# Kernel optimization log

Hardware: AMD Instinct MI355X
Metric: run time of the kernel (lower is better)

Reference implementation:

```python
import jax, jax.numpy as jnp
import numpy as np

EPS = 1e-5
GROUPS = 8
OUT_PLANES = 256
GP = OUT_PLANES // GROUPS  # group_planes = 32


def _bn_eval(x, p, ch_axis):
    # p: [4, C] = (gamma, beta, running_mean, running_var); eval-mode batchnorm
    shape = [1] * x.ndim
    shape[ch_axis] = -1
    g, b, m, v = (p[i].reshape(shape) for i in range(4))
    return g * (x - m) * jax.lax.rsqrt(v + EPS) + b


def _make_bn(key, ch):
    k1, k2, k3, k4 = jax.random.split(key, 4)
    gamma = jax.random.uniform(k1, (ch,)) + 0.5
    beta = jax.random.normal(k2, (ch,)) * 0.1
    mean = jax.random.normal(k3, (ch,)) * 0.1
    var = jax.random.uniform(k4, (ch,)) + 0.5
    return jnp.stack([gamma, beta, mean, var])  # [4, ch]


def setup_inputs() -> dict:
    key = jax.random.key(0)
    ks = jax.random.split(key, 6)
    N, C, D, Hh, Ww = 1, 256, 16, 32, 64
    x = jax.random.normal(ks[0], (N, C, D, Hh, Ww), dtype=jnp.float32)
    # qkv 1x1 conv weight: [out_planes*2, in_planes]
    qkv_w = jax.random.normal(ks[1], (OUT_PLANES * 2, C), dtype=jnp.float32) * np.sqrt(1.0 / C)
    # relative positional table: [group_planes*2, 2*H-1]
    relative = jax.random.normal(ks[2], (GP * 2, 2 * Ww - 1), dtype=jnp.float32) * np.sqrt(1.0 / GP)
    bn_qkv = _make_bn(ks[3], OUT_PLANES * 2)
    bn_sim = _make_bn(ks[4], GROUPS * 3)
    bn_out = _make_bn(ks[5], OUT_PLANES * 2)
    return {"x": x, "qkv_w": qkv_w, "relative": relative,
            "bn_qkv": bn_qkv, "bn_sim": bn_sim, "bn_out": bn_out}


def reference(x, qkv_w, relative, bn_qkv, bn_sim, bn_out):
    N, C, D, Hh, Ww = x.shape
    G, OP, gp = GROUPS, OUT_PLANES, GP
    # width == 0: permute(0,2,3,1,4) -> [N, D, Hh, C, Ww]; attend along Ww
    xp = jnp.transpose(x, (0, 2, 3, 1, 4))
    H = Ww
    B = N * D * Hh
    xr = xp.reshape(B, C, H)
    # 1x1 conv + BN over channels
    qkv = jnp.einsum('oc,bch->boh', qkv_w, xr)
    qkv = _bn_eval(qkv, bn_qkv, 1)
    qkv = qkv.reshape(B, G, 2 * gp, H)
    q = qkv[:, :, : gp // 2]          # [B,G,gp/2,H]
    k = qkv[:, :, gp // 2: gp]        # [B,G,gp/2,H]
    v = qkv[:, :, gp:]                # [B,G,gp,H]
    # relative-position gather: emb[c,i,j] = relative[c, i-j+H-1]
    idx = jnp.arange(H)[:, None] - jnp.arange(H)[None, :] + H - 1  # [H,H]
    emb = relative[:, idx]            # [2*gp, H, H]
    q_e = emb[: gp // 2]
    k_e = emb[gp // 2: gp]
    v_e = emb[gp:]
    qr = jnp.einsum('bgci,cij->bgij', q, q_e)
    kr = jnp.einsum('bgci,cij->bgji', k, k_e)  # einsum + transpose(2,3) fused
    qk = jnp.einsum('bgci,bgcj->bgij', q, k)
    sim = jnp.concatenate([qk, qr, kr], axis=1)  # [B, 3G, H, H]
    sim = _bn_eval(sim, bn_sim, 1)
    sim = sim.reshape(B, 3, G, H, H).sum(axis=1)
    sim = jax.nn.softmax(sim, axis=3)
    sv = jnp.einsum('bgij,bgcj->bgci', sim, v)
    sve = jnp.einsum('bgij,cij->bgci', sim, v_e)
    so = jnp.concatenate([sv, sve], axis=-1).reshape(B, 2 * OP, H)
    out = _bn_eval(so, bn_out, 1)
    out = out.reshape(N, D, Hh, OP, 2, H).sum(axis=-2)
    out = jnp.transpose(out, (0, 3, 1, 2, 4))  # [N, OP, D, Hh, Ww]
    return out
```

## Files before the change

### kernel.cpp

```cpp
#include <hip/hip_runtime.h>

#define EPS 1e-5f

typedef _Float16 half4_t __attribute__((ext_vector_type(4)));
typedef _Float16 half8_t __attribute__((ext_vector_type(8)));
typedef float floatx4 __attribute__((ext_vector_type(4)));

__device__ __forceinline__ unsigned short f2hb(float f) {
  _Float16 h = (_Float16)f;
  return __builtin_bit_cast(unsigned short, h);
}
__device__ __forceinline__ float hb2f(unsigned short u) {
  return (float)__builtin_bit_cast(_Float16, u);
}
__device__ __forceinline__ unsigned int pack2(float a, float b) {
  return (unsigned int)f2hb(a) | ((unsigned int)f2hb(b) << 16);
}

#define WS_QKT 16777216
#define WS_WH 33554432
#define WS_RELTQ 33816576
#define WS_RELTK 33820672
#define WS_RELV 33824768
#define WS_BNSF 33832960
#define WS_BNOSC 33833088
#define WS_BNOSH 33835136
#define WS_BNQSC 33837184
#define WS_BNQSH 33839232

__global__ __launch_bounds__(256) void k_prep(const float* __restrict__ W,
                                              const float* __restrict__ bnq,
                                              const float* __restrict__ rel,
                                              const float* __restrict__ bns,
                                              const float* __restrict__ bno,
                                              char* __restrict__ ws) {
  const int bid = blockIdx.x, tid = threadIdx.x;
  if (bid < 8) {
    unsigned short* Wh = (unsigned short*)(ws + WS_WH);
    const int base = bid * 16384;
#pragma unroll
    for (int u = 0; u < 16; ++u) {
      const int i = base + u * 1024 + tid * 4;
      const float4 v = *reinterpret_cast<const float4*>(&W[i]);
      uint2 p;
      p.x = pack2(v.x, v.y);
      p.y = pack2(v.z, v.w);
      *reinterpret_cast<uint2*>(&Wh[i]) = p;
    }
  } else {
    unsigned short* relTq = (unsigned short*)(ws + WS_RELTQ);
    unsigned short* relTk = (unsigned short*)(ws + WS_RELTK);
    unsigned short* relV = (unsigned short*)(ws + WS_RELV);
    float* bnsF = (float*)(ws + WS_BNSF);
    float* bnoSc = (float*)(ws + WS_BNOSC);
    float* bnoSh = (float*)(ws + WS_BNOSH);
    float* bnqSc = (float*)(ws + WS_BNQSC);
    float* bnqSh = (float*)(ws + WS_BNQSH);
    for (int idx = tid; idx < 2048; idx += 256) {
      const int t = idx >> 4, c = idx & 15;
      relTq[idx] = (t < 127) ? f2hb(rel[c * 127 + t]) : (unsigned short)0;
      relTk[idx] = (t < 127) ? f2hb(rel[(16 + c) * 127 + t]) : (unsigned short)0;
    }
    for (int idx = tid; idx < 4096; idx += 256) {
      const int c = idx >> 7, t = idx & 127;
      relV[idx] = (t < 127) ? f2hb(rel[(32 + c) * 127 + t]) : (unsigned short)0;
    }
    if (tid < 8) {
      const int g = tid;
      const float scA = bns[g] / sqrtf(bns[72 + g] + EPS);
      const float scB = bns[8 + g] / sqrtf(bns[72 + 8 + g] + EPS);
      const float scC = bns[16 + g] / sqrtf(bns[72 + 16 + g] + EPS);
      const float shv = (bns[24 + g] - bns[48 + g] * scA) +
                        (bns[24 + 8 + g] - bns[48 + 8 + g] * scB) +
                        (bns[24 + 16 + g] - bns[48 + 16 + g] * scC);
      bnsF[g * 4 + 0] = scA;
      bnsF[g * 4 + 1] = scB;
      bnsF[g * 4 + 2] = scC;
      bnsF[g * 4 + 3] = shv;
    }
    for (int idx = tid; idx < 512; idx += 256) {
      const float sc = bno[idx] / sqrtf(bno[1536 + idx] + EPS);
      bnoSc[idx] = sc;
      bnoSh[idx] = bno[512 + idx] - bno[1024 + idx] * sc;
      const float qc = bnq[idx] / sqrtf(bnq[1536 + idx] + EPS);
      bnqSc[idx] = qc;
      bnqSh[idx] = bnq[512 + idx] - bnq[1024 + idx] * qc;
    }
  }
}

__global__ __launch_bounds__(512, 4) void k_qkv(const float* __restrict__ x,
                                                char* __restrict__ ws) {
  const unsigned short* Wh = (const unsigned short*)(ws + WS_WH);
  const float* bnqSc = (const float*)(ws + WS_BNQSC);
  const float* bnqSh = (const float*)(ws + WS_BNQSH);
  unsigned short* qkv_h = (unsigned short*)ws;
  unsigned short* qkT = (unsigned short*)(ws + WS_QKT);
  __shared__ __align__(16) char arena[36864];
  unsigned short* xT = (unsigned short*)arena;
  unsigned short* qk_t = (unsigned short*)arena;

  const int tid = threadIdx.x;
  const int lane = tid & 63;
  const int w = tid >> 6;
  const int l15 = lane & 15, kg = lane >> 4;
  const size_t b = blockIdx.x;
  const int n0g = (int)b * 64;

  {
    const int k = tid >> 1;
    const int nb = (tid & 1) * 32;
    const float* src = x + (size_t)k * 32768 + n0g + nb;
    unsigned short hv[32];
#pragma unroll
    for (int u = 0; u < 8; ++u) {
      const float4 v4 = *reinterpret_cast<const float4*>(src + u * 4);
      hv[u * 4 + 0] = f2hb(v4.x);
      hv[u * 4 + 1] = f2hb(v4.y);
      hv[u * 4 + 2] = f2hb(v4.z);
      hv[u * 4 + 3] = f2hb(v4.w);
    }
#pragma unroll
    for (int e = 0; e < 32; ++e) xT[(nb + e) * 280 + k] = hv[e];
  }
  __syncthreads();

  floatx4 acc[4][4] = {};
#pragma unroll
  for (int kk = 0; kk < 8; ++kk) {
    half8_t af[4], bf[4];
#pragma unroll
    for (int fm = 0; fm < 4; ++fm)
      af[fm] = *reinterpret_cast<const half8_t*>(Wh + (size_t)(w * 64 + fm * 16 + l15) * 256 +
                                                 kk * 32 + kg * 8);
#pragma unroll
    for (int fn = 0; fn < 4; ++fn)
      bf[fn] = *reinterpret_cast<const half8_t*>(xT + (fn * 16 + l15) * 280 + kk * 32 + kg * 8);
#pragma unroll
    for (int fm = 0; fm < 4; ++fm)
#pragma unroll
      for (int fn = 0; fn < 4; ++fn)
        acc[fm][fn] = __builtin_amdgcn_mfma_f32_16x16x32_f16(af[fm], bf[fn], acc[fm][fn], 0, 0, 0);
  }
  __syncthreads();

  const int o0 = w * 64;
#pragma unroll
  for (int fm = 0; fm < 4; ++fm) {
    const float4 sc4 = *reinterpret_cast<const float4*>(&bnqSc[o0 + fm * 16 + kg * 4]);
    const float4 sh4 = *reinterpret_cast<const float4*>(&bnqSh[o0 + fm * 16 + kg * 4]);
#pragma unroll
    for (int fn = 0; fn < 4; ++fn) {
      const int h = fn * 16 + l15;
      const float v0 = fmaf(acc[fm][fn][0], sc4.x, sh4.x);
      const float v1 = fmaf(acc[fm][fn][1], sc4.y, sh4.y);
      const float v2 = fmaf(acc[fm][fn][2], sc4.z, sh4.z);
      const float v3 = fmaf(acc[fm][fn][3], sc4.w, sh4.w);
      if (fm < 2) {
        uint2 p;
        p.x = pack2(v0, v1);
        p.y = pack2(v2, v3);
        *reinterpret_cast<uint2*>(&qk_t[w * 2304 + h * 36 + fm * 16 + kg * 4]) = p;
      } else {
        const int cb = (fm - 2) * 16 + kg * 4;
        unsigned short* dst = &qkv_h[((b * 8 + w) * 32 + cb) * 64 + h];
        dst[0] = f2hb(v0);
        dst[64] = f2hb(v1);
        dst[128] = f2hb(v2);
        dst[192] = f2hb(v3);
      }
    }
  }
  __syncthreads();
#pragma unroll
  for (int it = 0; it < 4; ++it) {
    const int idx = it * 512 + tid;
    const int g2 = idx >> 8, e = idx & 255;
    const int h = e >> 2, c0 = (e & 3) * 8;
    const unsigned short* srcp = &qk_t[g2 * 2304 + h * 36 + c0];
    const uint2 a = *reinterpret_cast<const uint2*>(srcp);
    const uint2 b2 = *reinterpret_cast<const uint2*>(srcp + 4);
    uint4 wv;
    wv.x = a.x;
    wv.y = a.y;
    wv.z = b2.x;
    wv.w = b2.y;
    *reinterpret_cast<uint4*>(&qkT[((b * 8 + g2) * 64 + h) * 32 + c0]) = wv;
  }
}

#define QKS 36
#define PBS 72
#define PPS 136

__global__ __launch_bounds__(256, 4) void k_attn(const char* __restrict__ ws,
                                                 float* __restrict__ out) {
  const unsigned short* qkv_h = (const unsigned short*)ws;
  const unsigned short* qkTg = (const unsigned short*)(ws + WS_QKT);
  const unsigned short* relTq = (const unsigned short*)(ws + WS_RELTQ);
  const unsigned short* relTk = (const unsigned short*)(ws + WS_RELTK);
  const unsigned short* relV = (const unsigned short*)(ws + WS_RELV);
  const float* bnsF = (const float*)(ws + WS_BNSF);
  const float* bnoSc = (const float*)(ws + WS_BNOSC);
  const float* bnoSh = (const float*)(ws + WS_BNOSH);

  __shared__ __align__(16) char arena[32768];
  unsigned short* qkL = (unsigned short*)arena;
  unsigned short* M1T = (unsigned short*)arena;
  unsigned short* M2T = (unsigned short*)(arena + 16384);
  unsigned short* Pb = (unsigned short*)arena;
  unsigned short* Pp = (unsigned short*)(arena + 9216);
  unsigned short* Vb = (unsigned short*)(arena + 26624);
  float* rowsumL = (float*)(arena + 31232);

  const int tid = threadIdx.x;
  const int lane = tid & 63;
  const int wid = tid >> 6;
  const int l15 = lane & 15, kg = lane >> 4;
  const int bg = blockIdx.x;
  const int b = bg >> 3, g = bg & 7;

  {
    const uint4 qv =
        *reinterpret_cast<const uint4*>(&qkTg[(size_t)(((b << 3) + g)) * 2048 + tid * 8]);
    const int i = tid >> 2, c0 = (tid & 3) * 8;
    uint2 lo, hi;
    lo.x = qv.x;
    lo.y = qv.y;
    hi.x = qv.z;
    hi.y = qv.w;
    *reinterpret_cast<uint2*>(&qkL[i * QKS + c0]) = lo;
    *reinterpret_cast<uint2*>(&qkL[i * QKS + c0 + 4]) = hi;
  }
  __syncthreads();

  const half4_t aq = *reinterpret_cast<const half4_t*>(&qkL[(wid * 16 + l15) * QKS + kg * 4]);
  const half4_t ak =
      *reinterpret_cast<const half4_t*>(&qkL[(wid * 16 + l15) * QKS + 16 + kg * 4]);
  half4_t bqr[4];
#pragma unroll
  for (int nt = 0; nt < 4; ++nt)
    bqr[nt] = *reinterpret_cast<const half4_t*>(&qkL[(nt * 16 + l15) * QKS + 16 + kg * 4]);
  __syncthreads();

  floatx4 qkreg[4];
  {
    half4_t brq[8], brk[8];
#pragma unroll
    for (int nt = 0; nt < 8; ++nt) {
      brq[nt] = *reinterpret_cast<const half4_t*>(&relTq[(nt * 16 + l15) * 16 + kg * 4]);
      brk[nt] = *reinterpret_cast<const half4_t*>(&relTk[(nt * 16 + l15) * 16 + kg * 4]);
    }
    __builtin_amdgcn_s_setprio(1);
#pragma unroll
    for (int nt = 0; nt < 4; ++nt) {
      const floatx4 z = {};
      qkreg[nt] = __builtin_amdgcn_mfma_f32_16x16x16f16(aq, bqr[nt], z, 0, 0, 0);
    }
    const int mcol = wid * 16 + kg * 4;
#pragma unroll
    for (int nt = 0; nt < 8; ++nt) {
      const floatx4 z = {};
      const floatx4 cr = __builtin_amdgcn_mfma_f32_16x16x16f16(aq, brq[nt], z, 0, 0, 0);
      const int row = nt * 16 + l15;
      uint2 p;
      p.x = pack2(cr[0], cr[1]);
      p.y = pack2(cr[2], cr[3]);
      *reinterpret_cast<uint2*>(&M1T[row * 64 + (mcol ^ ((row & 7) << 3))]) = p;
    }
#pragma unroll
    for (int nt = 0; nt < 8; ++nt) {
      const floatx4 z = {};
      const floatx4 cr = __builtin_amdgcn_mfma_f32_16x16x16f16(ak, brk[nt], z, 0, 0, 0);
      const int row = nt * 16 + l15;
      uint2 p;
      p.x = pack2(cr[0], cr[1]);
      p.y = pack2(cr[2], cr[3]);
      *reinterpret_cast<uint2*>(&M2T[row * 64 + (mcol ^ ((row & 7) << 3))]) = p;
    }
    __builtin_amdgcn_s_setprio(0);
  }
  __syncthreads();

  const uint4 vld = *reinterpret_cast<const uint4*>(
      &qkv_h[(((size_t)b * 8 + g) * 32 + (tid >> 3)) * 64 + (tid & 7) * 8]);
  float sreg[4][4];
  {
    const float4 bf = *reinterpret_cast<const float4*>(&bnsF[g * 4]);
#pragma unroll
    for (int nt = 0; nt < 4; ++nt) {
      const int j = nt * 16 + l15;
#pragma unroll
      for (int r = 0; r < 4; ++r) {
        const int i = wid * 16 + kg * 4 + r;
        const int d = i - j + 63;
        const int d2 = 126 - d;
        const float qr = hb2f(M1T[d * 64 + (i ^ ((d & 7) << 3))]);
        const float kr = hb2f(M2T[d2 * 64 + (j ^ ((d2 & 7) << 3))]);
        sreg[nt][r] = fmaf(bf.x, qkreg[nt][r], fmaf(bf.y, qr, fmaf(bf.z, kr, bf.w)));
      }
    }
  }
  __syncthreads();

  float sm[4];
#pragma unroll
  for (int r = 0; r < 4; ++r) {
    float m = fmaxf(fmaxf(sreg[0][r], sreg[1][r]), fmaxf(sreg[2][r], sreg[3][r]));
    m = fmaxf(m, __shfl_xor(m, 1));
    m = fmaxf(m, __shfl_xor(m, 2));
    m = fmaxf(m, __shfl_xor(m, 4));
    m = fmaxf(m, __shfl_xor(m, 8));
    float s = 0.f;
#pragma unroll
    for (int nt = 0; nt < 4; ++nt) {
      sreg[nt][r] = __expf(sreg[nt][r] - m);
      s += sreg[nt][r];
    }
    s += __shfl_xor(s, 1);
    s += __shfl_xor(s, 2);
    s += __shfl_xor(s, 4);
    s += __shfl_xor(s, 8);
    sm[r] = s;
  }
#pragma unroll
  for (int r = 0; r < 4; ++r) {
    const int i = wid * 16 + kg * 4 + r;
    const int z0 = l15 * 4;
    if (z0 + 3 < i) {
      uint2 zz;
      zz.x = 0u;
      zz.y = 0u;
      *reinterpret_cast<uint2*>(&Pp[i * PPS + z0]) = zz;
    } else if (z0 >= i) {
      uint2 zz;
      zz.x = 0u;
      zz.y = 0u;
      *reinterpret_cast<uint2*>(&Pp[i * PPS + z0 + 64]) = zz;
    } else {
#pragma unroll
      for (int e = 0; e < 4; ++e) {
        const int z = z0 + e;
        Pp[i * PPS + (z < i ? z : z + 64)] = 0;
      }
    }
#pragma unroll
    for (int nt = 0; nt < 4; ++nt) {
      const int j = nt * 16 + l15;
      const unsigned short pv = f2hb(sreg[nt][r]);
      Pb[i * PBS + j] = pv;
      Pp[i * PPS + i + 63 - j] = pv;
    }
    if (l15 == 0) rowsumL[i] = sm[r];
  }
  {
    *reinterpret_cast<uint4*>(&Vb[(tid >> 3) * PBS + (tid & 7) * 8]) = vld;
  }
  __syncthreads();

  floatx4 sva[2] = {}, svea[2] = {};
  __builtin_amdgcn_s_setprio(1);
#pragma unroll
  for (int kk = 0; kk < 2; ++kk) {
    const half8_t pbf =
        *reinterpret_cast<const half8_t*>(&Pb[(wid * 16 + l15) * PBS + kk * 32 + kg * 8]);
#pragma unroll
    for (int cf = 0; cf < 2; ++cf) {
      const half8_t vb =
          *reinterpret_cast<const half8_t*>(&Vb[(cf * 16 + l15) * PBS + kk * 32 + kg * 8]);
      sva[cf] = __builtin_amdgcn_mfma_f32_16x16x32_f16(vb, pbf, sva[cf], 0, 0, 0);
    }
  }
#pragma unroll
  for (int kk = 0; kk < 4; ++kk) {
    const half8_t ppf =
        *reinterpret_cast<const half8_t*>(&Pp[(wid * 16 + l15) * PPS + kk * 32 + kg * 8]);
#pragma unroll
    for (int cf = 0; cf < 2; ++cf) {
      const half8_t rb =
          *reinterpret_cast<const half8_t*>(&relV[(cf * 16 + l15) * 128 + kk * 32 + kg * 8]);
      svea[cf] = __builtin_amdgcn_mfma_f32_16x16x32_f16(rb, ppf, svea[cf], 0, 0, 0);
    }
  }
  __builtin_amdgcn_s_setprio(0);
  {
    const int i = wid * 16 + l15;
    const float inv = 1.0f / rowsumL[i];
#pragma unroll
    for (int cf = 0; cf < 2; ++cf) {
#pragma unroll
      for (int reg = 0; reg < 4; ++reg) {
        const int c = cf * 16 + kg * 4 + reg;
        const int ch = ((g << 5) + c) * 2;
        const float2 scv = *reinterpret_cast<const float2*>(&bnoSc[ch]);
        const float2 shv = *reinterpret_cast<const float2*>(&bnoSh[ch]);
        out[(size_t)((g << 5) + c) * 32768 + (size_t)b * 64 + i] =
            fmaf(scv.x, sva[cf][reg] * inv, shv.x) + fmaf(scv.y, svea[cf][reg] * inv, shv.y);
      }
    }
  }
}

extern "C" void kernel_launch(void* const* d_in, const int* in_sizes, int n_in,
                              void* d_out, int out_size, void* d_ws, size_t ws_size,
                              hipStream_t stream) {
  const float* x = (const float*)d_in[0];
  const float* qkv_w = (const float*)d_in[1];
  const float* relative = (const float*)d_in[2];
  const float* bn_qkv = (const float*)d_in[3];
  const float* bn_sim = (const float*)d_in[4];
  const float* bn_out = (const float*)d_in[5];
  float* out = (float*)d_out;
  char* ws = (char*)d_ws;

  k_prep<<<9, 256, 0, stream>>>(qkv_w, bn_qkv, relative, bn_sim, bn_out, ws);
  k_qkv<<<512, 512, 0, stream>>>(x, ws);
  k_attn<<<4096, 256, 0, stream>>>(ws, out);
}
```

Measured before the change: 80.69 us.

## Process two (batch,group) tiles per attention block with upfront global loads

Each k_attn block now handles two consecutive (b,g) pairs in a loop, issuing the global loads for both pairs' q/k and v data at the start so later loads overlap with compute. The LDS arena grows so the qk staging area no longer aliases the M1T/Pb regions, and the grid is halved. This aims to hide global load latency and amortize block launch cost, at the price of more registers, more shared memory per block and possibly lower occupancy.

```diff
diff --git a/kernel.cpp b/kernel.cpp
--- a/kernel.cpp
+++ b/kernel.cpp
@@ -204,198 +204,208 @@
   const float* bnoSc = (const float*)(ws + WS_BNOSC);
   const float* bnoSh = (const float*)(ws + WS_BNOSH);
 
-  __shared__ __align__(16) char arena[32768];
+  __shared__ __align__(16) char arena[37376];
   unsigned short* qkL = (unsigned short*)arena;
-  unsigned short* M1T = (unsigned short*)arena;
-  unsigned short* M2T = (unsigned short*)(arena + 16384);
-  unsigned short* Pb = (unsigned short*)arena;
-  unsigned short* Pp = (unsigned short*)(arena + 9216);
-  unsigned short* Vb = (unsigned short*)(arena + 26624);
-  float* rowsumL = (float*)(arena + 31232);
+  unsigned short* M1T = (unsigned short*)(arena + 4608);
+  unsigned short* M2T = (unsigned short*)(arena + 20992);
+  unsigned short* Pb = (unsigned short*)(arena + 4608);
+  unsigned short* Pp = (unsigned short*)(arena + 13824);
+  unsigned short* Vb = (unsigned short*)(arena + 31232);
+  float* rowsumL = (float*)(arena + 35840);
 
   const int tid = threadIdx.x;
   const int lane = tid & 63;
   const int wid = tid >> 6;
   const int l15 = lane & 15, kg = lane >> 4;
-  const int bg = blockIdx.x;
-  const int b = bg >> 3, g = bg & 7;
-
-  {
-    const uint4 qv =
-        *reinterpret_cast<const uint4*>(&qkTg[(size_t)(((b << 3) + g)) * 2048 + tid * 8]);
-    const int i = tid >> 2, c0 = (tid & 3) * 8;
-    uint2 lo, hi;
-    lo.x = qv.x;
-    lo.y = qv.y;
-    hi.x = qv.z;
-    hi.y = qv.w;
-    *reinterpret_cast<uint2*>(&qkL[i * QKS + c0]) = lo;
-    *reinterpret_cast<uint2*>(&qkL[i * QKS + c0 + 4]) = hi;
-  }
-  __syncthreads();
-
-  const half4_t aq = *reinterpret_cast<const half4_t*>(&qkL[(wid * 16 + l15) * QKS + kg * 4]);
-  const half4_t ak =
-      *reinterpret_cast<const half4_t*>(&qkL[(wid * 16 + l15) * QKS + 16 + kg * 4]);
-  half4_t bqr[4];
-#pragma unroll
-  for (int nt = 0; nt < 4; ++nt)
-    bqr[nt] = *reinterpret_cast<const half4_t*>(&qkL[(nt * 16 + l15) * QKS + 16 + kg * 4]);
-  __syncthreads();
-
-  floatx4 qkreg[4];
-  {
-    half4_t brq[8], brk[8];
-#pragma unroll
-    for (int nt = 0; nt < 8; ++nt) {
-      brq[nt] = *reinterpret_cast<const half4_t*>(&relTq[(nt * 16 + l15) * 16 + kg * 4]);
-      brk[nt] = *reinterpret_cast<const half4_t*>(&relTk[(nt * 16 + l15) * 16 + kg * 4]);
-    }
+  const size_t idx0 = (size_t)blockIdx.x * 2;
+
+  const uint4 qvA = *reinterpret_cast<const uint4*>(&qkTg[idx0 * 2048 + tid * 8]);
+  const uint4 qvB = *reinterpret_cast<const uint4*>(&qkTg[(idx0 + 1) * 2048 + tid * 8]);
+  const uint4 vlA = *reinterpret_cast<const uint4*>(
+      &qkv_h[(idx0 * 32 + (tid >> 3)) * 64 + (tid & 7) * 8]);
+  const uint4 vlB = *reinterpret_cast<const uint4*>(
+      &qkv_h[((idx0 + 1) * 32 + (tid >> 3)) * 64 + (tid & 7) * 8]);
+
+#pragma unroll
+  for (int p = 0; p < 2; ++p) {
+    const size_t idx = idx0 + p;
+    const int b = (int)(idx >> 3), g = (int)(idx & 7);
+    const uint4 qv = (p == 0) ? qvA : qvB;
+    const uint4 vld = (p == 0) ? vlA : vlB;
+
+    {
+      const int i = tid >> 2, c0 = (tid & 3) * 8;
+      uint2 lo, hi;
+      lo.x = qv.x;
+      lo.y = qv.y;
+      hi.x = qv.z;
+      hi.y = qv.w;
+      *reinterpret_cast<uint2*>(&qkL[i * QKS + c0]) = lo;
+      *reinterpret_cast<uint2*>(&qkL[i * QKS + c0 + 4]) = hi;
+    }
+    __syncthreads();
+
+    const half4_t aq = *reinterpret_cast<const half4_t*>(&qkL[(wid * 16 + l15) * QKS + kg * 4]);
+    const half4_t ak =
+        *reinterpret_cast<const half4_t*>(&qkL[(wid * 16 + l15) * QKS + 16 + kg * 4]);
+    half4_t bqr[4];
+#pragma unroll
+    for (int nt = 0; nt < 4; ++nt)
+      bqr[nt] = *reinterpret_cast<const half4_t*>(&qkL[(nt * 16 + l15) * QKS + 16 + kg * 4]);
+    __syncthreads();
+
+    floatx4 qkreg[4];
+    {
+      half4_t brq[8], brk[8];
+#pragma unroll
+      for (int nt = 0; nt < 8; ++nt) {
+        brq[nt] = *reinterpret_cast<const half4_t*>(&relTq[(nt * 16 + l15) * 16 + kg * 4]);
+        brk[nt] = *reinterpret_cast<const half4_t*>(&relTk[(nt * 16 + l15) * 16 + kg * 4]);
+      }
+      __builtin_amdgcn_s_setprio(1);
+#pragma unroll
+      for (int nt = 0; nt < 4; ++nt) {
+        const floatx4 z = {};
+        qkreg[nt] = __builtin_amdgcn_mfma_f32_16x16x16f16(aq, bqr[nt], z, 0, 0, 0);
+      }
+      const int mcol = wid * 16 + kg * 4;
+#pragma unroll
+      for (int nt = 0; nt < 8; ++nt) {
+        const floatx4 z = {};
+        const floatx4 cr = __builtin_amdgcn_mfma_f32_16x16x16f16(aq, brq[nt], z, 0, 0, 0);
+        const int row = nt * 16 + l15;
+        uint2 pq;
+        pq.x = pack2(cr[0], cr[1]);
+        pq.y = pack2(cr[2], cr[3]);
+        *reinterpret_cast<uint2*>(&M1T[row * 64 + (mcol ^ ((row & 7) << 3))]) = pq;
+      }
+#pragma unroll
+      for (int nt = 0; nt < 8; ++nt) {
+        const floatx4 z = {};
+        const floatx4 cr = __builtin_amdgcn_mfma_f32_16x16x16f16(ak, brk[nt], z, 0, 0, 0);
+        const int row = nt * 16 + l15;
+        uint2 pq;
+        pq.x = pack2(cr[0], cr[1]);
+        pq.y = pack2(cr[2], cr[3]);
+        *reinterpret_cast<uint2*>(&M2T[row * 64 + (mcol ^ ((row & 7) << 3))]) = pq;
+      }
+      __builtin_amdgcn_s_setprio(0);
+    }
+    __syncthreads();
+
+    float sreg[4][4];
+    {
+      const float4 bf = *reinterpret_cast<const float4*>(&bnsF[g * 4]);
+#pragma unroll
+      for (int nt = 0; nt < 4; ++nt) {
+        const int j = nt * 16 + l15;
+#pragma unroll
+        for (int r = 0; r < 4; ++r) {
+          const int i = wid * 16 + kg * 4 + r;
+          const int d = i - j + 63;
+          const int d2 = 126 - d;
+          const float qr = hb2f(M1T[d * 64 + (i ^ ((d & 7) << 3))]);
+          const float kr = hb2f(M2T[d2 * 64 + (j ^ ((d2 & 7) << 3))]);
+          sreg[nt][r] = fmaf(bf.x, qkreg[nt][r], fmaf(bf.y, qr, fmaf(bf.z, kr, bf.w)));
+        }
+      }
+    }
+    __syncthreads();
+
+    float sm[4];
+#pragma unroll
+    for (int r = 0; r < 4; ++r) {
+      float m = fmaxf(fmaxf(sreg[0][r], sreg[1][r]), fmaxf(sreg[2][r], sreg[3][r]));
+      m = fmaxf(m, __shfl_xor(m, 1));
+      m = fmaxf(m, __shfl_xor(m, 2));
+      m = fmaxf(m, __shfl_xor(m, 4));
+      m = fmaxf(m, __shfl_xor(m, 8));
+      float s = 0.f;
+#pragma unroll
+      for (int nt = 0; nt < 4; ++nt) {
+        sreg[nt][r] = __expf(sreg[nt][r] - m);
+        s += sreg[nt][r];
+      }
+      s += __shfl_xor(s, 1);
+      s += __shfl_xor(s, 2);
+      s += __shfl_xor(s, 4);
+      s += __shfl_xor(s, 8);
+      sm[r] = s;
+    }
+#pragma unroll
+    for (int r = 0; r < 4; ++r) {
+      const int i = wid * 16 + kg * 4 + r;
+      const int z0 = l15 * 4;
+      if (z0 + 3 < i) {
+        uint2 zz;
+        zz.x = 0u;
+        zz.y = 0u;
+        *reinterpret_cast<uint2*>(&Pp[i * PPS + z0]) = zz;
+      } else if (z0 >= i) {
+        uint2 zz;
+        zz.x = 0u;
+        zz.y = 0u;
+        *reinterpret_cast<uint2*>(&Pp[i * PPS + z0 + 64]) = zz;
+      } else {
+#pragma unroll
+        for (int e = 0; e < 4; ++e) {
+          const int z = z0 + e;
+          Pp[i * PPS + (z < i ? z : z + 64)] = 0;
+        }
+      }
+#pragma unroll
+      for (int nt = 0; nt < 4; ++nt) {
+        const int j = nt * 16 + l15;
+        const unsigned short pv = f2hb(sreg[nt][r]);
+        Pb[i * PBS + j] = pv;
+        Pp[i * PPS + i + 63 - j] = pv;
+      }
+      if (l15 == 0) rowsumL[i] = sm[r];
+    }
+    {
+      *reinterpret_cast<uint4*>(&Vb[(tid >> 3) * PBS + (tid & 7) * 8]) = vld;
+    }
+    __syncthreads();
+
+    floatx4 sva[2] = {}, svea[2] = {};
     __builtin_amdgcn_s_setprio(1);
 #pragma unroll
-    for (int nt = 0; nt < 4; ++nt) {
-      const floatx4 z = {};
-      qkreg[nt] = __builtin_amdgcn_mfma_f32_16x16x16f16(aq, bqr[nt], z, 0, 0, 0);
-    }
-    const int mcol = wid * 16 + kg * 4;
-#pragma unroll
-    for (int nt = 0; nt < 8; ++nt) {
-      const floatx4 z = {};
-      const floatx4 cr = __builtin_amdgcn_mfma_f32_16x16x16f16(aq, brq[nt], z, 0, 0, 0);
-      const int row = nt * 16 + l15;
-      uint2 p;
-      p.x = pack2(cr[0], cr[1]);
-      p.y = pack2(cr[2], cr[3]);
-      *reinterpret_cast<uint2*>(&M1T[row * 64 + (mcol ^ ((row & 7) << 3))]) = p;
-    }
-#pragma unroll
-    for (int nt = 0; nt < 8; ++nt) {
-      const floatx4 z = {};
-      const floatx4 cr = __builtin_amdgcn_mfma_f32_16x16x16f16(ak, brk[nt], z, 0, 0, 0);
-      const int row = nt * 16 + l15;
-      uint2 p;
-      p.x = pack2(cr[0], cr[1]);
-      p.y = pack2(cr[2], cr[3]);
-      *reinterpret_cast<uint2*>(&M2T[row * 64 + (mcol ^ ((row & 7) << 3))]) = p;
+    for (int kk = 0; kk < 2; ++kk) {
+      const half8_t pbf =
+          *reinterpret_cast<const half8_t*>(&Pb[(wid * 16 + l15) * PBS + kk * 32 + kg * 8]);
+#pragma unroll
+      for (int cf = 0; cf < 2; ++cf) {
+        const half8_t vb =
+            *reinterpret_cast<const half8_t*>(&Vb[(cf * 16 + l15) * PBS + kk * 32 + kg * 8]);
+        sva[cf] = __builtin_amdgcn_mfma_f32_16x16x32_f16(vb, pbf, sva[cf], 0, 0, 0);
+      }
+    }
+#pragma unroll
+    for (int kk = 0; kk < 4; ++kk) {
+      const half8_t ppf =
+          *reinterpret_cast<const half8_t*>(&Pp[(wid * 16 + l15) * PPS + kk * 32 + kg * 8]);
+#pragma unroll
+      for (int cf = 0; cf < 2; ++cf) {
+        const half8_t rb =
+            *reinterpret_cast<const half8_t*>(&relV[(cf * 16 + l15) * 128 + kk * 32 + kg * 8]);
+        svea[cf] = __builtin_amdgcn_mfma_f32_16x16x32_f16(rb, ppf, svea[cf], 0, 0, 0);
+      }
     }
     __builtin_amdgcn_s_setprio(0);
-  }
-  __syncthreads();
-
-  const uint4 vld = *reinterpret_cast<const uint4*>(
-      &qkv_h[(((size_t)b * 8 + g) * 32 + (tid >> 3)) * 64 + (tid & 7) * 8]);
-  float sreg[4][4];
-  {
-    const float4 bf = *reinterpret_cast<const float4*>(&bnsF[g * 4]);
-#pragma unroll
-    for (int nt = 0; nt < 4; ++nt) {
-      const int j = nt * 16 + l15;
-#pragma unroll
-      for (int r = 0; r < 4; ++r) {
-        const int i = wid * 16 + kg * 4 + r;
-        const int d = i - j + 63;
-        const int d2 = 126 - d;
-        const float qr = hb2f(M1T[d * 64 + (i ^ ((d & 7) << 3))]);
-        const float kr = hb2f(M2T[d2 * 64 + (j ^ ((d2 & 7) << 3))]);
-        sreg[nt][r] = fmaf(bf.x, qkreg[nt][r], fmaf(bf.y, qr, fmaf(bf.z, kr, bf.w)));
-      }
-    }
-  }
-  __syncthreads();
-
-  float sm[4];
-#pragma unroll
-  for (int r = 0; r < 4; ++r) {
-    float m = fmaxf(fmaxf(sreg[0][r], sreg[1][r]), fmaxf(sreg[2][r], sreg[3][r]));
-    m = fmaxf(m, __shfl_xor(m, 1));
-    m = fmaxf(m, __shfl_xor(m, 2));
-    m = fmaxf(m, __shfl_xor(m, 4));
-    m = fmaxf(m, __shfl_xor(m, 8));
-    float s = 0.f;
-#pragma unroll
-    for (int nt = 0; nt < 4; ++nt) {
-      sreg[nt][r] = __expf(sreg[nt][r] - m);
-      s += sreg[nt][r];
-    }
-    s += __shfl_xor(s, 1);
-    s += __shfl_xor(s, 2);
-    s += __shfl_xor(s, 4);
-    s += __shfl_xor(s, 8);
-    sm[r] = s;
-  }
-#pragma unroll
-  for (int r = 0; r < 4; ++r) {
-    const int i = wid * 16 + kg * 4 + r;
-    const int z0 = l15 * 4;
-    if (z0 + 3 < i) {
-      uint2 zz;
-      zz.x = 0u;
-      zz.y = 0u;
-      *reinterpret_cast<uint2*>(&Pp[i * PPS + z0]) = zz;
-    } else if (z0 >= i) {
-      uint2 zz;
-      zz.x = 0u;
-      zz.y = 0u;
-      *reinterpret_cast<uint2*>(&Pp[i * PPS + z0 + 64]) = zz;
-    } else {
-#pragma unroll
-      for (int e = 0; e < 4; ++e) {
-        const int z = z0 + e;
-        Pp[i * PPS + (z < i ? z : z + 64)] = 0;
-      }
-    }
-#pragma unroll
-    for (int nt = 0; nt < 4; ++nt) {
-      const int j = nt * 16 + l15;
-      const unsigned short pv = f2hb(sreg[nt][r]);
-      Pb[i * PBS + j] = pv;
-      Pp[i * PPS + i + 63 - j] = pv;
-    }
-    if (l15 == 0) rowsumL[i] = sm[r];
-  }
-  {
-    *reinterpret_cast<uint4*>(&Vb[(tid >> 3) * PBS + (tid & 7) * 8]) = vld;
-  }
-  __syncthreads();
-
-  floatx4 sva[2] = {}, svea[2] = {};
-  __builtin_amdgcn_s_setprio(1);
-#pragma unroll
-  for (int kk = 0; kk < 2; ++kk) {
-    const half8_t pbf =
-        *reinterpret_cast<const half8_t*>(&Pb[(wid * 16 + l15) * PBS + kk * 32 + kg * 8]);
-#pragma unroll
-    for (int cf = 0; cf < 2; ++cf) {
-      const half8_t vb =
-          *reinterpret_cast<const half8_t*>(&Vb[(cf * 16 + l15) * PBS + kk * 32 + kg * 8]);
-      sva[cf] = __builtin_amdgcn_mfma_f32_16x16x32_f16(vb, pbf, sva[cf], 0, 0, 0);
-    }
-  }
-#pragma unroll
-  for (int kk = 0; kk < 4; ++kk) {
-    const half8_t ppf =
-        *reinterpret_cast<const half8_t*>(&Pp[(wid * 16 + l15) * PPS + kk * 32 + kg * 8]);
-#pragma unroll
-    for (int cf = 0; cf < 2; ++cf) {
-      const half8_t rb =
-          *reinterpret_cast<const half8_t*>(&relV[(cf * 16 + l15) * 128 + kk * 32 + kg * 8]);
-      svea[cf] = __builtin_amdgcn_mfma_f32_16x16x32_f16(rb, ppf, svea[cf], 0, 0, 0);
-    }
-  }
-  __builtin_amdgcn_s_setprio(0);
-  {
-    const int i = wid * 16 + l15;
-    const float inv = 1.0f / rowsumL[i];
-#pragma unroll
-    for (int cf = 0; cf < 2; ++cf) {
-#pragma unroll
-      for (int reg = 0; reg < 4; ++reg) {
-        const int c = cf * 16 + kg * 4 + reg;
-        const int ch = ((g << 5) + c) * 2;
-        const float2 scv = *reinterpret_cast<const float2*>(&bnoSc[ch]);
-        const float2 shv = *reinterpret_cast<const float2*>(&bnoSh[ch]);
-        out[(size_t)((g << 5) + c) * 32768 + (size_t)b * 64 + i] =
-            fmaf(scv.x, sva[cf][reg] * inv, shv.x) + fmaf(scv.y, svea[cf][reg] * inv, shv.y);
+    {
+      const int i = wid * 16 + l15;
+      const float inv = 1.0f / rowsumL[i];
+#pragma unroll
+      for (int cf = 0; cf < 2; ++cf) {
+#pragma unroll
+        for (int reg = 0; reg < 4; ++reg) {
+          const int c = cf * 16 + kg * 4 + reg;
+          const int ch = ((g << 5) + c) * 2;
+          const float2 scv = *reinterpret_cast<const float2*>(&bnoSc[ch]);
+          const float2 shv = *reinterpret_cast<const float2*>(&bnoSh[ch]);
+          out[(size_t)((g << 5) + c) * 32768 + (size_t)b * 64 + i] =
+              fmaf(scv.x, sva[cf][reg] * inv, shv.x) + fmaf(scv.y, svea[cf][reg] * inv, shv.y);
+        }
       }
     }
   }
@@ -415,5 +425,5 @@
 
   k_prep<<<9, 256, 0, stream>>>(qkv_w, bn_qkv, relative, bn_sim, bn_out, ws);
   k_qkv<<<512, 512, 0, stream>>>(x, ws);
-  k_attn<<<4096, 256, 0, stream>>>(ws, out);
-}
+  k_attn<<<2048, 256, 0, stream>>>(ws, out);
+}
```

After: 87.56 us. +8.5%, slower.
